# Kernel tuning notes

Measured on AMD Instinct MI355X. Metric: run time of the kernel, lower is better.

The kernel has to match this reference:

```python
import jax, jax.numpy as jnp
import numpy as np

N = 16384        # total atoms
E = 262144       # edges
D = 128          # dim_embedding
F = 128          # num_filters
G = 50           # num_gaussians
L = 4            # num_interactions
CUTOFF = 5.0
GAMMA = 4.0
NUM_MOLS = 32
LOG2 = float(np.log(2.0))


def ssp(x):
    # ShiftedSoftplus: softplus(x) - log(2)
    return jax.nn.softplus(x) - LOG2


def setup_inputs() -> dict:
    key = jax.random.key(0)
    ks = jax.random.split(key, 24)
    s = lambda *sh: 1.0 / np.sqrt(sh[-2]) if len(sh) >= 2 else 0.1
    inp = {
        "z": jax.random.normal(ks[0], (N, 1), jnp.float32),
        "pos": jax.random.uniform(ks[1], (N, 3), jnp.float32),
        "batch": jnp.sort(jax.random.randint(ks[2], (N,), 0, NUM_MOLS)),
        "edge_src": jax.random.randint(ks[3], (E,), 0, N),
        "edge_dst": jax.random.randint(ks[4], (E,), 0, N),
        # embedding Linear(1, D)
        "emb_W": jax.random.normal(ks[5], (1, D), jnp.float32),
        "emb_b": jax.random.normal(ks[6], (D,), jnp.float32) * 0.1,
        # per-interaction stacked params [L, ...]
        "mlp_W1": jax.random.normal(ks[7], (L, G, F), jnp.float32) / np.sqrt(G),
        "mlp_b1": jnp.zeros((L, F), jnp.float32),
        "mlp_W2": jax.random.normal(ks[8], (L, F, F), jnp.float32) / np.sqrt(F),
        "mlp_b2": jnp.zeros((L, F), jnp.float32),
        "cf1_W": jax.random.normal(ks[9], (L, D, F), jnp.float32) / np.sqrt(D),   # CFConv.lin1 (no bias)
        "cf2_W": jax.random.normal(ks[10], (L, F, D), jnp.float32) / np.sqrt(F),  # CFConv.lin2
        "cf2_b": jnp.zeros((L, D), jnp.float32),
        "int_lin_W": jax.random.normal(ks[11], (L, D, D), jnp.float32) / np.sqrt(D),
        "int_lin_b": jnp.zeros((L, D), jnp.float32),
        # readout head
        "lin1_W": jax.random.normal(ks[12], (D, D // 2), jnp.float32) / np.sqrt(D),
        "lin1_b": jnp.zeros((D // 2,), jnp.float32),
        "lin2_W": jax.random.normal(ks[13], (D // 2, 1), jnp.float32) / np.sqrt(D // 2),
        "lin2_b": jnp.zeros((1,), jnp.float32),
    }
    return inp


def reference(z, pos, batch, edge_src, edge_dst, emb_W, emb_b,
              mlp_W1, mlp_b1, mlp_W2, mlp_b2, cf1_W, cf2_W, cf2_b,
              int_lin_W, int_lin_b, lin1_W, lin1_b, lin2_W, lin2_b):
    # atom embedding: Linear(1, D)
    h = z @ emb_W + emb_b                                  # [N, D]

    # interaction graph distances (graph connectivity precomputed)
    diff = pos[edge_src] - pos[edge_dst]                   # [E, 3]
    dist = jnp.sqrt(jnp.sum(diff * diff, axis=-1) + 1e-12) # [E]

    # radial basis expansion
    mu = jnp.linspace(0.0, CUTOFF, G).astype(h.dtype)      # [G]
    rbf = jnp.exp(-GAMMA * (dist[:, None] - mu) ** 2)      # [E, G]

    # cosine cutoff envelope
    C = 0.5 * (jnp.cos(dist * (np.pi / CUTOFF)) + 1.0)     # [E]

    for l in range(L):
        # continuous filter from RBF: MLP [E,G] -> [E,F]
        Wf = ssp(rbf @ mlp_W1[l] + mlp_b1[l]) @ mlp_W2[l] + mlp_b2[l]
        Wf = Wf * C[:, None]                               # [E, F]
        # CFConv: gather - multiply - scatter-add
        xj = (h @ cf1_W[l])[edge_src]                      # [E, F]
        agg = jax.ops.segment_sum(xj * Wf, edge_dst, num_segments=N)  # [N, F]
        x = agg @ cf2_W[l] + cf2_b[l]                      # [N, D]
        x = ssp(x)
        x = x @ int_lin_W[l] + int_lin_b[l]
        h = h + x                                          # residual

    h = ssp(h @ lin1_W + lin1_b) @ lin2_W + lin2_b         # [N, 1]
    out = jax.ops.segment_sum(h, batch, num_segments=NUM_MOLS)  # [NUM_MOLS, 1]
    return out
```

## Files before the change

### kernel.cpp

```cpp
#include <hip/hip_runtime.h>
#include <hip/hip_bf16.h>
#include <math.h>

#define N_ATOMS 16384
#define N_EDGES 262144
#define DIM 128
#define NF 128
#define NG 50
#define NL 4
#define NMOLS 32
#define EW 8
#define EB 4

typedef short bf16x8 __attribute__((ext_vector_type(8)));
typedef float f32x4 __attribute__((ext_vector_type(4)));

__device__ __forceinline__ float ssp_f(float x) {
    float e = __expf(-fabsf(x));
    return fmaxf(x, 0.0f) + __logf(1.0f + e) - 0.6931471805599453f;
}

__device__ __forceinline__ short f2bf(float x) {
    __hip_bfloat16 b = __float2bfloat16(x);
    return *reinterpret_cast<short*>(&b);
}

__device__ __forceinline__ float bf2f(unsigned short u) {
    unsigned int v = ((unsigned int)u) << 16;
    return __builtin_bit_cast(float, v);
}

__global__ void k_embed(const float* __restrict__ z, const float* __restrict__ Wv,
                        const float* __restrict__ bv, float* __restrict__ h) {
    int idx = blockIdx.x * blockDim.x + threadIdx.x;
    int n = idx >> 7, d = idx & 127;
    h[idx] = z[n] * Wv[d] + bv[d];
}

__global__ void k_geom(const float* __restrict__ pos, const int* __restrict__ src,
                       const int* __restrict__ dst, float* __restrict__ dist,
                       float* __restrict__ Cenv) {
    int e = blockIdx.x * blockDim.x + threadIdx.x;
    if (e >= N_EDGES) return;
    int s = src[e], t = dst[e];
    float dx = pos[3*s]   - pos[3*t];
    float dy = pos[3*s+1] - pos[3*t+1];
    float dz = pos[3*s+2] - pos[3*t+2];
    float d = sqrtf(dx*dx + dy*dy + dz*dz + 1e-12f);
    dist[e] = d;
    Cenv[e] = 0.5f * (cosf(d * (float)(M_PI / 5.0)) + 1.0f);
}

__global__ void k_deg(const int* __restrict__ dst, int* __restrict__ deg) {
    int e = blockIdx.x * blockDim.x + threadIdx.x;
    if (e < N_EDGES) atomicAdd(&deg[dst[e]], 1);
}

__global__ __launch_bounds__(1024)
void k_scan(const int* __restrict__ deg, int* __restrict__ cur) {
    __shared__ int tot[1024];
    int t = threadIdx.x;
    int v[16];
    int s = 0;
    #pragma unroll
    for (int j = 0; j < 16; ++j) { int x = deg[t * 16 + j]; v[j] = s; s += x; }
    tot[t] = s;
    __syncthreads();
    for (int off = 1; off < 1024; off <<= 1) {
        int add = (t >= off) ? tot[t - off] : 0;
        __syncthreads();
        tot[t] += add;
        __syncthreads();
    }
    int base = (t == 0) ? 0 : tot[t - 1];
    #pragma unroll
    for (int j = 0; j < 16; ++j) cur[t * 16 + j] = base + v[j];
}

__global__ void k_fill(const int* __restrict__ dst, int* __restrict__ cur,
                       int* __restrict__ edge_of) {
    int e = blockIdx.x * blockDim.x + threadIdx.x;
    if (e < N_EDGES) {
        int p = atomicAdd(&cur[dst[e]], 1);
        edge_of[p] = e;
    }
}

__global__ void k_perm(const int* __restrict__ edge_of, const float* __restrict__ dist,
                       const float* __restrict__ Cenv, const int* __restrict__ src,
                       const int* __restrict__ dst, float* __restrict__ distS,
                       float* __restrict__ CenvS, int* __restrict__ srcS,
                       int* __restrict__ dstS) {
    int p = blockIdx.x * blockDim.x + threadIdx.x;
    if (p >= N_EDGES) return;
    int e = edge_of[p];
    distS[p] = dist[e];
    CenvS[p] = Cenv[e];
    srcS[p]  = src[e];
    dstS[p]  = dst[e];
}

__global__ __launch_bounds__(512)
void k_rbf(const float* __restrict__ distS, short* __restrict__ rbfF) {
    int lane = threadIdx.x & 63;
    int w    = threadIdx.x >> 6;
    int t    = blockIdx.x * 8 + w;
    int q = lane >> 4, m = lane & 15;
    float d = distS[t * 16 + m];
    #pragma unroll
    for (int kc = 0; kc < 2; ++kc) {
        bf16x8 v;
        #pragma unroll
        for (int j = 0; j < 8; ++j) {
            float mu = (float)(kc * 32 + q * 8 + j) * (5.0f / 49.0f);
            float tt = d - mu;
            v[j] = f2bf(__expf(-4.0f * tt * tt));
        }
        *(bf16x8*)&rbfF[(size_t)((t * 2 + kc) * 64 + lane) * 8] = v;
    }
}

__global__ __launch_bounds__(512, 4)
void k_edge_csr(const short* __restrict__ rbfF, const float* __restrict__ CenvS,
                const int* __restrict__ srcS, const int* __restrict__ dstS,
                const float* __restrict__ W1, const float* __restrict__ b1,
                const float* __restrict__ W2, const float* __restrict__ b2,
                const unsigned short* __restrict__ xjb, float* __restrict__ agg)
{
    __shared__ short H1s[64 * 128];
    __shared__ unsigned short msgt[64][136];
    __shared__ int dsts[64];
    __shared__ unsigned long long maskS;
    const int tid  = threadIdx.x;
    const int lane = tid & 63;
    const int w    = tid >> 6;
    const int q    = lane >> 4;
    const int m    = lane & 15;

    bf16x8 W1R[2], W2R[4];
    #pragma unroll
    for (int kc = 0; kc < 2; ++kc) {
        bf16x8 f;
        #pragma unroll
        for (int j = 0; j < 8; ++j) {
            int k = kc * 32 + q * 8 + j;
            float v = (k < NG) ? W1[k * NF + w * 16 + m] : 0.0f;
            f[j] = f2bf(v);
        }
        W1R[kc] = f;
    }
    #pragma unroll
    for (int kc = 0; kc < 4; ++kc) {
        bf16x8 f;
        #pragma unroll
        for (int j = 0; j < 8; ++j) {
            int k = kc * 32 + q * 8 + j;
            f[j] = f2bf(W2[k * NF + w * 16 + m]);
        }
        W2R[kc] = f;
    }
    const float b1v = b1[w * 16 + m];
    const float b2v = b2[w * 16 + m];

    const int nrounds = N_EDGES / 64;
    for (int r = blockIdx.x; r < nrounds; r += gridDim.x) {
        const int p0 = r * 64;
        short* H = H1s;

        #pragma unroll
        for (int a = 0; a < 4; ++a) {
            int tile = r * 4 + a;
            f32x4 acc = {b1v, b1v, b1v, b1v};
            #pragma unroll
            for (int kc = 0; kc < 2; ++kc) {
                bf16x8 A = *(const bf16x8*)&rbfF[(size_t)((tile * 2 + kc) * 64 + lane) * 8];
                acc = __builtin_amdgcn_mfma_f32_16x16x32_bf16(A, W1R[kc], acc, 0, 0, 0);
            }
            #pragma unroll
            for (int i = 0; i < 4; ++i) {
                int e = a * 16 + q * 4 + i;
                int f = w * 16 + m;
                int byte = (e * 256 + f * 2) ^ ((e & 7) << 4);
                *(short*)((char*)H + byte) = f2bf(ssp_f(acc[i]));
            }
        }
        __syncthreads();

        unsigned short xu[4][4];
        #pragma unroll
        for (int a = 0; a < 4; ++a) {
            int4 s4 = *(const int4*)&srcS[p0 + a * 16 + q * 4];
            #pragma unroll
            for (int i = 0; i < 4; ++i)
                xu[a][i] = xjb[(size_t)((const int*)&s4)[i] * NF + w * 16 + m];
        }

        f32x4 acc2[4];
        #pragma unroll
        for (int a = 0; a < 4; ++a) {
            f32x4 acc = {b2v, b2v, b2v, b2v};
            #pragma unroll
            for (int kc = 0; kc < 4; ++kc) {
                int e = a * 16 + m;
                int byte = (e * 256 + (kc * 32 + q * 8) * 2) ^ ((e & 7) << 4);
                bf16x8 A = *(const bf16x8*)((const char*)H + byte);
                acc = __builtin_amdgcn_mfma_f32_16x16x32_bf16(A, W2R[kc], acc, 0, 0, 0);
            }
            acc2[a] = acc;
        }

        #pragma unroll
        for (int a = 0; a < 4; ++a) {
            float4 cc4 = *(const float4*)&CenvS[p0 + a * 16 + q * 4];
            #pragma unroll
            for (int i = 0; i < 4; ++i) {
                float v = acc2[a][i] * ((const float*)&cc4)[i];
                msgt[a * 16 + q * 4 + i][w * 16 + m] =
                    (unsigned short)f2bf(v * bf2f(xu[a][i]));
            }
        }
        if (w == 0) {
            int d = dstS[p0 + lane];
            int prev = __shfl_up(d, 1);
            bool head = (lane == 0) || (d != prev);
            unsigned long long mk = __ballot(head);
            dsts[lane] = d;
            if (lane == 0) maskS = mk;
        }
        __syncthreads();

        {
            int f = tid & 127;
            int g = tid >> 7;
            unsigned long long mm = maskS;
            int k = 0;
            while (mm) {
                int start = __ffsll(mm) - 1;
                mm &= mm - 1;
                int end = mm ? (__ffsll(mm) - 1) : 64;
                if ((k & 3) == g) {
                    float s = 0.0f;
                    for (int p = start; p < end; ++p) s += bf2f(msgt[p][f]);
                    float* addr = &agg[(size_t)dsts[start] * NF + f];
                    if (start == 0 || end == 64) atomicAdd(addr, s);
                    else *addr = s;
                }
                ++k;
            }
        }
    }
}

template<int ACT, int RESID, int OUTBF>
__global__ __launch_bounds__(512, 2)
void k_node_mfma(const float* __restrict__ in, const float* __restrict__ W,
                 const float* __restrict__ bias, const float* __restrict__ resid,
                 void* __restrict__ outv)
{
    __shared__ short T[64 * 128];
    const int tid  = threadIdx.x;
    const int lane = tid & 63;
    const int w    = tid >> 6;
    const int q    = lane >> 4;
    const int m    = lane & 15;

    bf16x8 WR[4];
    #pragma unroll
    for (int kc = 0; kc < 4; ++kc) {
        bf16x8 f;
        #pragma unroll
        for (int j = 0; j < 8; ++j)
            f[j] = f2bf(W[(kc * 32 + q * 8 + j) * DIM + w * 16 + m]);
        WR[kc] = f;
    }
    const float bv = bias ? bias[w * 16 + m] : 0.0f;

    const int r0 = blockIdx.x * 64;

    {
        int row = tid >> 3;
        int k0  = (tid & 7) * 16;
        const float* src = in + (size_t)(r0 + row) * DIM + k0;
        float4 v0 = *(const float4*)(src);
        float4 v1 = *(const float4*)(src + 4);
        float4 v2 = *(const float4*)(src + 8);
        float4 v3 = *(const float4*)(src + 12);
        bf16x8 lo, hi;
        #pragma unroll
        for (int j = 0; j < 4; ++j) {
            lo[j]     = f2bf(((const float*)&v0)[j]);
            lo[j + 4] = f2bf(((const float*)&v1)[j]);
            hi[j]     = f2bf(((const float*)&v2)[j]);
            hi[j + 4] = f2bf(((const float*)&v3)[j]);
        }
        int b0 = (row * 256 + k0 * 2)       ^ ((row & 7) << 4);
        int b1 = (row * 256 + (k0 + 8) * 2) ^ ((row & 7) << 4);
        *(bf16x8*)((char*)T + b0) = lo;
        *(bf16x8*)((char*)T + b1) = hi;
    }
    __syncthreads();

    #pragma unroll
    for (int a = 0; a < 4; ++a) {
        f32x4 acc = {bv, bv, bv, bv};
        int row = a * 16 + m;
        #pragma unroll
        for (int kc = 0; kc < 4; ++kc) {
            int byte = (row * 256 + (kc * 32 + q * 8) * 2) ^ ((row & 7) << 4);
            bf16x8 A = *(const bf16x8*)((const char*)T + byte);
            acc = __builtin_amdgcn_mfma_f32_16x16x32_bf16(A, WR[kc], acc, 0, 0, 0);
        }
        #pragma unroll
        for (int i = 0; i < 4; ++i) {
            float v = acc[i];
            if (ACT) v = ssp_f(v);
            size_t oi = (size_t)(r0 + a * 16 + q * 4 + i) * DIM + w * 16 + m;
            if (RESID) v += ((const float*)outv == nullptr ? 0.0f : resid[oi]);
            if (OUTBF) ((unsigned short*)outv)[oi] = (unsigned short)f2bf(v);
            else       ((float*)outv)[oi] = v;
        }
    }
}

template<int COLS, int ACT, int RESID>
__global__ __launch_bounds__(512)
void k_node_gemm(const float* __restrict__ in, const float* __restrict__ W,
                 const float* __restrict__ bias, const float* __restrict__ resid,
                 float* __restrict__ out)
{
    __shared__ float Ws[DIM][COLS];
    __shared__ float rs[EW][EB][DIM];
    int tid = threadIdx.x;
    for (int i = tid; i < DIM * COLS; i += 512) (&Ws[0][0])[i] = W[i];
    __syncthreads();

    int lane = tid & 63;
    int w = tid >> 6;
    int gw = blockIdx.x * EW + w;
    int nw = gridDim.x * EW;
    int ngroups = N_ATOMS / EB;
    constexpr int CPL = COLS / 64;

    float bb[CPL];
    #pragma unroll
    for (int c = 0; c < CPL; ++c) bb[c] = bias ? bias[lane + 64 * c] : 0.0f;

    for (int grp = gw; grp < ngroups; grp += nw) {
        int r0 = grp * EB;
        #pragma unroll
        for (int r = 0; r < EB; ++r) {
            rs[w][r][lane]      = in[(size_t)(r0 + r) * DIM + lane];
            rs[w][r][lane + 64] = in[(size_t)(r0 + r) * DIM + lane + 64];
        }
        float acc[EB][CPL];
        #pragma unroll
        for (int r = 0; r < EB; ++r)
            #pragma unroll
            for (int c = 0; c < CPL; ++c) acc[r][c] = bb[c];
        #pragma unroll 2
        for (int kb = 0; kb < DIM / 4; ++kb) {
            float4 rv[EB];
            #pragma unroll
            for (int r = 0; r < EB; ++r)
                rv[r] = *(const float4*)&rs[w][r][4 * kb];
            #pragma unroll
            for (int j = 0; j < 4; ++j) {
                float wv[CPL];
                #pragma unroll
                for (int c = 0; c < CPL; ++c) wv[c] = Ws[4 * kb + j][lane + 64 * c];
                #pragma unroll
                for (int r = 0; r < EB; ++r) {
                    float rj = ((const float*)&rv[r])[j];
                    #pragma unroll
                    for (int c = 0; c < CPL; ++c)
                        acc[r][c] = fmaf(rj, wv[c], acc[r][c]);
                }
            }
        }
        #pragma unroll
        for (int r = 0; r < EB; ++r) {
            #pragma unroll
            for (int c = 0; c < CPL; ++c) {
                float v = acc[r][c];
                if (ACT) v = ssp_f(v);
                size_t oi = (size_t)(r0 + r) * COLS + lane + 64 * c;
                if (RESID) v += resid[oi];
                out[oi] = v;
            }
        }
    }
}

__global__ __launch_bounds__(256)
void k_final(const float* __restrict__ r1, const float* __restrict__ l2W,
             const float* __restrict__ l2b, const int* __restrict__ batch,
             float* __restrict__ out)
{
    __shared__ float mols[NMOLS];
    int tid = threadIdx.x;
    if (tid < NMOLS) mols[tid] = 0.0f;
    __syncthreads();

    int n = blockIdx.x * 256 + tid;
    const float4* row = (const float4*)(r1 + (size_t)n * 64);
    const float4* wv  = (const float4*)l2W;
    float s = 0.0f;
    #pragma unroll
    for (int k = 0; k < 16; ++k) {
        float4 a = row[k], b = wv[k];
        s += a.x * b.x + a.y * b.y + a.z * b.z + a.w * b.w;
    }
    s += l2b[0];
    atomicAdd(&mols[batch[n]], s);
    __syncthreads();
    if (tid < NMOLS) atomicAdd(&out[tid], mols[tid]);
}

extern "C" void kernel_launch(void* const* d_in, const int* in_sizes, int n_in,
                              void* d_out, int out_size, void* d_ws, size_t ws_size,
                              hipStream_t stream) {
    const float* z     = (const float*)d_in[0];
    const float* pos   = (const float*)d_in[1];
    const int*   batch = (const int*)d_in[2];
    const int*   esrc  = (const int*)d_in[3];
    const int*   edst  = (const int*)d_in[4];
    const float* embW  = (const float*)d_in[5];
    const float* embB  = (const float*)d_in[6];
    const float* mlpW1 = (const float*)d_in[7];
    const float* mlpB1 = (const float*)d_in[8];
    const float* mlpW2 = (const float*)d_in[9];
    const float* mlpB2 = (const float*)d_in[10];
    const float* cf1W  = (const float*)d_in[11];
    const float* cf2W  = (const float*)d_in[12];
    const float* cf2B  = (const float*)d_in[13];
    const float* intW  = (const float*)d_in[14];
    const float* intB  = (const float*)d_in[15];
    const float* l1W   = (const float*)d_in[16];
    const float* l1B   = (const float*)d_in[17];
    const float* l2W   = (const float*)d_in[18];
    const float* l2B   = (const float*)d_in[19];
    float* out = (float*)d_out;

    char* ws = (char*)d_ws;
    float* h     = (float*)(ws);
    float* dist  = (float*)(ws + (size_t)( 8 << 20));
    float* Cv    = (float*)(ws + (size_t)( 9 << 20));
    unsigned short* xj = (unsigned short*)(ws + (size_t)(10 << 20));
    float* tbuf  = (float*)(ws + (size_t)(10 << 20));
    float* agg   = (float*)(ws + (size_t)(18 << 20));
    short* rbfF  = (short*)(ws + (size_t)(26 << 20));
    int*   deg   = (int*)  (ws + (size_t)(58 << 20));
    int*   cur   = (int*)  (ws + (size_t)(59 << 20));
    int*   edge_of = (int*)(ws + (size_t)(60 << 20));
    float* distS = (float*)(ws + (size_t)(61 << 20));
    float* CenvS = (float*)(ws + (size_t)(62 << 20));
    int*   srcS  = (int*)  (ws + (size_t)(63 << 20));
    int*   dstS  = (int*)  (ws + (size_t)(64 << 20));
    float* r1    = agg;

    k_embed<<<dim3(N_ATOMS * DIM / 512), dim3(512), 0, stream>>>(z, embW, embB, h);
    k_geom<<<dim3(N_EDGES / 256), dim3(256), 0, stream>>>(pos, esrc, edst, dist, Cv);

    hipMemsetAsync(deg, 0, N_ATOMS * sizeof(int), stream);
    k_deg<<<dim3(N_EDGES / 512), dim3(512), 0, stream>>>(edst, deg);
    k_scan<<<dim3(1), dim3(1024), 0, stream>>>(deg, cur);
    k_fill<<<dim3(N_EDGES / 512), dim3(512), 0, stream>>>(edst, cur, edge_of);
    k_perm<<<dim3(N_EDGES / 512), dim3(512), 0, stream>>>(edge_of, dist, Cv, esrc, edst,
                                                          distS, CenvS, srcS, dstS);
    k_rbf<<<dim3(N_EDGES / 16 / 8), dim3(512), 0, stream>>>(distS, rbfF);

    for (int l = 0; l < NL; ++l) {
        k_node_mfma<0, 0, 1><<<dim3(N_ATOMS / 64), dim3(512), 0, stream>>>(
            h, cf1W + (size_t)l * DIM * NF, nullptr, nullptr, (void*)xj);
        hipMemsetAsync(agg, 0, (size_t)N_ATOMS * NF * sizeof(float), stream);
        k_edge_csr<<<dim3(1024), dim3(512), 0, stream>>>(
            rbfF, CenvS, srcS, dstS,
            mlpW1 + (size_t)l * NG * NF, mlpB1 + (size_t)l * NF,
            mlpW2 + (size_t)l * NF * NF, mlpB2 + (size_t)l * NF,
            xj, agg);
        k_node_mfma<1, 0, 0><<<dim3(N_ATOMS / 64), dim3(512), 0, stream>>>(
            agg, cf2W + (size_t)l * NF * DIM, cf2B + (size_t)l * DIM, nullptr, (void*)tbuf);
        k_node_mfma<0, 1, 0><<<dim3(N_ATOMS / 64), dim3(512), 0, stream>>>(
            tbuf, intW + (size_t)l * DIM * DIM, intB + (size_t)l * DIM, h, (void*)h);
    }

    k_node_gemm<64, 1, 0><<<dim3(256), dim3(512), 0, stream>>>(h, l1W, l1B, nullptr, r1);
    hipMemsetAsync(out, 0, NMOLS * sizeof(float), stream);
    k_final<<<dim3(N_ATOMS / 256), dim3(256), 0, stream>>>(r1, l2W, l2B, batch, out);
}
```

Measured before the change: 526.6 us.

## Segment-reduce edge messages with a selection-matrix MFMA and double-buffer H1

Within each 64-edge round, the sorted-by-destination segment sum is now done as an MFMA. A 0/1 selection matrix built from the run-head ballot mask is multiplied by the message tile, with a scalar fallback when a round has more than 16 runs. Each warp now computes the dst run mask itself, which removes the separate warp-0 stage. H1 is double-buffered so one of the two block barriers per round can be dropped. The grid is reduced from 1024 to 768 blocks, and a redundant null check in the residual path is removed. The msgt column reads are strided and the grid change is a tuning guess.

```diff
diff --git a/kernel.cpp b/kernel.cpp
--- a/kernel.cpp
+++ b/kernel.cpp
@@ -127,10 +127,9 @@
                 const float* __restrict__ W2, const float* __restrict__ b2,
                 const unsigned short* __restrict__ xjb, float* __restrict__ agg)
 {
-    __shared__ short H1s[64 * 128];
+    __shared__ short H1s[2][64 * 128];
     __shared__ unsigned short msgt[64][136];
-    __shared__ int dsts[64];
-    __shared__ unsigned long long maskS;
+    __shared__ int dsthW[EW][16];
     const int tid  = threadIdx.x;
     const int lane = tid & 63;
     const int w    = tid >> 6;
@@ -163,9 +162,10 @@
     const float b2v = b2[w * 16 + m];
 
     const int nrounds = N_EDGES / 64;
-    for (int r = blockIdx.x; r < nrounds; r += gridDim.x) {
+    int rb = 0;
+    for (int r = blockIdx.x; r < nrounds; r += gridDim.x, ++rb) {
         const int p0 = r * 64;
-        short* H = H1s;
+        short* H = H1s[rb & 1];
 
         #pragma unroll
         for (int a = 0; a < 4; ++a) {
@@ -184,7 +184,6 @@
                 *(short*)((char*)H + byte) = f2bf(ssp_f(acc[i]));
             }
         }
-        __syncthreads();
 
         unsigned short xu[4][4];
         #pragma unroll
@@ -194,6 +193,17 @@
             for (int i = 0; i < 4; ++i)
                 xu[a][i] = xjb[(size_t)((const int*)&s4)[i] * NF + w * 16 + m];
         }
+        int dstv = dstS[p0 + lane];
+        int prev = __shfl_up(dstv, 1);
+        bool head = (lane == 0) || (dstv != prev);
+        unsigned long long mk = __ballot(head);
+        int nruns = __popcll(mk);
+        {
+            int rid = __popcll(mk & ((1ull << lane) - 1ull));
+            if (head && rid < 16) dsthW[w][rid] = dstv;
+        }
+
+        __syncthreads();
 
         f32x4 acc2[4];
         #pragma unroll
@@ -219,29 +229,51 @@
                     (unsigned short)f2bf(v * bf2f(xu[a][i]));
             }
         }
-        if (w == 0) {
-            int d = dstS[p0 + lane];
-            int prev = __shfl_up(d, 1);
-            bool head = (lane == 0) || (d != prev);
-            unsigned long long mk = __ballot(head);
-            dsts[lane] = d;
-            if (lane == 0) maskS = mk;
-        }
-        __syncthreads();
-
-        {
-            int f = tid & 127;
-            int g = tid >> 7;
-            unsigned long long mm = maskS;
+
+        if (nruns <= 16) {
+            bf16x8 Mf[2];
+            #pragma unroll
+            for (int kc = 0; kc < 2; ++kc) {
+                bf16x8 t;
+                #pragma unroll
+                for (int j = 0; j < 8; ++j)
+                    t[j] = (short)msgt[kc * 32 + q * 8 + j][w * 16 + m];
+                Mf[kc] = t;
+            }
+            f32x4 D = {0.0f, 0.0f, 0.0f, 0.0f};
+            #pragma unroll
+            for (int kc = 0; kc < 2; ++kc) {
+                bf16x8 S;
+                #pragma unroll
+                for (int j = 0; j < 8; ++j) {
+                    int s = kc * 32 + q * 8 + j;
+                    unsigned long long pm = (2ull << s) - 1ull;
+                    int rid = __popcll(mk & pm) - 1;
+                    S[j] = (rid == m) ? (short)0x3F80 : (short)0;
+                }
+                D = __builtin_amdgcn_mfma_f32_16x16x32_bf16(S, Mf[kc], D, 0, 0, 0);
+            }
+            #pragma unroll
+            for (int i = 0; i < 4; ++i) {
+                int rr = q * 4 + i;
+                if (rr < nruns) {
+                    float* addr = &agg[(size_t)dsthW[w][rr] * NF + w * 16 + m];
+                    if (rr == 0 || rr == nruns - 1) atomicAdd(addr, D[i]);
+                    else *addr = D[i];
+                }
+            }
+        } else {
+            unsigned long long mm = mk;
             int k = 0;
             while (mm) {
                 int start = __ffsll(mm) - 1;
                 mm &= mm - 1;
                 int end = mm ? (__ffsll(mm) - 1) : 64;
-                if ((k & 3) == g) {
+                int dstart = __shfl(dstv, start);
+                if ((k & 3) == q) {
                     float s = 0.0f;
-                    for (int p = start; p < end; ++p) s += bf2f(msgt[p][f]);
-                    float* addr = &agg[(size_t)dsts[start] * NF + f];
+                    for (int p = start; p < end; ++p) s += bf2f(msgt[p][w * 16 + m]);
+                    float* addr = &agg[(size_t)dstart * NF + w * 16 + m];
                     if (start == 0 || end == 64) atomicAdd(addr, s);
                     else *addr = s;
                 }
@@ -315,7 +347,7 @@
             float v = acc[i];
             if (ACT) v = ssp_f(v);
             size_t oi = (size_t)(r0 + a * 16 + q * 4 + i) * DIM + w * 16 + m;
-            if (RESID) v += ((const float*)outv == nullptr ? 0.0f : resid[oi]);
+            if (RESID) v += resid[oi];
             if (OUTBF) ((unsigned short*)outv)[oi] = (unsigned short)f2bf(v);
             else       ((float*)outv)[oi] = v;
         }
@@ -473,7 +505,7 @@
         k_node_mfma<0, 0, 1><<<dim3(N_ATOMS / 64), dim3(512), 0, stream>>>(
             h, cf1W + (size_t)l * DIM * NF, nullptr, nullptr, (void*)xj);
         hipMemsetAsync(agg, 0, (size_t)N_ATOMS * NF * sizeof(float), stream);
-        k_edge_csr<<<dim3(1024), dim3(512), 0, stream>>>(
+        k_edge_csr<<<dim3(768), dim3(512), 0, stream>>>(
             rbfF, CenvS, srcS, dstS,
             mlpW1 + (size_t)l * NG * NF, mlpB1 + (size_t)l * NF,
             mlpW2 + (size_t)l * NF * NF, mlpB2 + (size_t)l * NF,
```

Measured after the change: 873.0 us. 65.8% more time.
